# Kernel tuning notes

Measured on AMD Instinct MI355X. Metric: run time of the kernel, lower is better.

Reference implementation:

```python
import jax, jax.numpy as jnp
import numpy as np

D_MODEL = 1024
D_STATE = 16
D_CONV = 4
EXPAND = 2
D_INNER = EXPAND * D_MODEL          # 2048
DT_RANK = D_MODEL // 16             # 64 (math.ceil(d_model/16))
BATCH, SEQLEN = 2, 1024


def setup_inputs() -> dict:
    key = jax.random.key(0)
    ks = jax.random.split(key, 9)
    f32 = jnp.float32
    hidden_states = jax.random.normal(ks[0], (BATCH, SEQLEN, D_MODEL), dtype=f32)
    in_proj_w = jax.random.normal(ks[1], (2 * D_INNER, D_MODEL), dtype=f32) * (D_MODEL ** -0.5)
    conv1d_w = jax.random.normal(ks[2], (D_INNER, D_CONV), dtype=f32) * (D_CONV ** -0.5)
    conv1d_b = jax.random.normal(ks[3], (D_INNER,), dtype=f32) * 0.1
    x_proj_w = jax.random.normal(ks[4], (DT_RANK + 2 * D_STATE, D_INNER), dtype=f32) * (D_INNER ** -0.5)
    dt_std = DT_RANK ** -0.5
    dt_proj_w = jax.random.uniform(ks[5], (D_INNER, DT_RANK), dtype=f32, minval=-dt_std, maxval=dt_std)
    dt_proj_b = jax.random.normal(ks[6], (D_INNER,), dtype=f32) * 0.1
    # A = repeat(arange(1, d_state+1), 'n -> d n'); A_log = log(A)
    A_log = jnp.log(jnp.tile(jnp.arange(1, D_STATE + 1, dtype=f32), (D_INNER, 1)))
    D_param = jnp.ones((D_INNER,), dtype=f32)
    out_proj_w = jax.random.normal(ks[7], (D_MODEL, D_INNER), dtype=f32) * (D_INNER ** -0.5)
    return dict(hidden_states=hidden_states, in_proj_w=in_proj_w, conv1d_w=conv1d_w,
                conv1d_b=conv1d_b, x_proj_w=x_proj_w, dt_proj_w=dt_proj_w,
                dt_proj_b=dt_proj_b, A_log=A_log, D_param=D_param, out_proj_w=out_proj_w)


def _mamba_fwd(hidden_states, in_proj_w, conv1d_w, conv1d_b, x_proj_w,
               dt_proj_w, dt_proj_b, A_log, D_param, out_proj_w):
    Bsz, L, _ = hidden_states.shape
    # in_proj: (B,L,d_model) -> (B,L,2*d_inner); split into x, z
    xz = jnp.einsum('bld,ed->ble', hidden_states, in_proj_w)
    x, z = jnp.split(xz, 2, axis=-1)                      # each (B,L,d_inner)
    # causal depthwise conv1d over L (left pad d_conv-1), then SiLU (fused in causal_conv1d_fwd)
    xc = jnp.transpose(x, (0, 2, 1))                      # (B,d_inner,L)
    kern = conv1d_w[:, None, :]                           # (d_inner,1,d_conv)
    conv = jax.lax.conv_general_dilated(
        xc, kern, window_strides=(1,), padding=[(D_CONV - 1, 0)],
        dimension_numbers=('NCH', 'OIH', 'NCH'), feature_group_count=D_INNER)
    u = jax.nn.silu(conv + conv1d_b[None, :, None])       # (B,d_inner,L)
    ut = jnp.transpose(u, (0, 2, 1))                      # (B,L,d_inner)
    # x_proj -> [dt | B | C]
    x_dbl = jnp.einsum('bld,rd->blr', ut, x_proj_w)       # (B,L,dt_rank+2*d_state)
    dt_low = x_dbl[..., :DT_RANK]
    B_var = x_dbl[..., DT_RANK:DT_RANK + D_STATE]         # (B,L,d_state)
    C_var = x_dbl[..., DT_RANK + D_STATE:]                # (B,L,d_state)
    # delta = softplus(dt_proj_w @ dt_low + dt_proj_b)  (delta_bias applied inside selective scan)
    delta = jax.nn.softplus(jnp.einsum('blr,dr->bld', dt_low, dt_proj_w) + dt_proj_b)  # (B,L,d_inner)
    A = -jnp.exp(A_log)                                   # (d_inner,d_state)
    # discretize: h_l = exp(delta*A) * h_{l-1} + (delta*B_l) * u_l
    dA = jnp.exp(delta[..., None] * A)                    # (B,L,d_inner,d_state)
    dBu = delta[..., None] * B_var[:, :, None, :] * ut[..., None]  # (B,L,d_inner,d_state)

    def step(h, inp):
        da, dbu, c = inp
        h = da * h + dbu                                  # (B,d_inner,d_state)
        y = jnp.einsum('bdn,bn->bd', h, c)
        return h, y

    h0 = jnp.zeros((Bsz, D_INNER, D_STATE), dtype=hidden_states.dtype)
    _, ys = jax.lax.scan(step, h0, (jnp.moveaxis(dA, 1, 0),
                                    jnp.moveaxis(dBu, 1, 0),
                                    jnp.moveaxis(C_var, 1, 0)))
    y = jnp.moveaxis(ys, 0, 1)                            # (B,L,d_inner)
    y = y + ut * D_param                                  # skip term D*u
    out_z = y * jax.nn.silu(z)                            # gated output
    return jnp.einsum('bld,ed->ble', out_z, out_proj_w)   # (B,L,d_model)


def reference(hidden_states, in_proj_w, conv1d_w, conv1d_b, x_proj_w,
              dt_proj_w, dt_proj_b, A_log, D_param, out_proj_w):
    return _mamba_fwd(hidden_states, in_proj_w, conv1d_w, conv1d_b, x_proj_w,
                      dt_proj_w, dt_proj_b, A_log, D_param, out_proj_w)
```

## Files before the change

kernel.cpp:

```cpp
#include <hip/hip_runtime.h>
#include <hip/hip_bf16.h>

#define BATCH 2
#define SEQLEN 1024
#define DMODEL 1024
#define DINNER 2048
#define DSTATE 16
#define DTRANK 64
#define ROWS (BATCH * SEQLEN)
#define LOG2E 1.44269504088896340736f

using bf16 = __hip_bfloat16;
typedef __bf16 bf16x8 __attribute__((ext_vector_type(8)));
typedef float f32x4 __attribute__((ext_vector_type(4)));
typedef unsigned short us8 __attribute__((ext_vector_type(8)));

__device__ __forceinline__ float to_f(float x) { return x; }
__device__ __forceinline__ float to_f(bf16 x) { return __bfloat162float(x); }

__device__ __forceinline__ float fexp2(float x) { return __builtin_amdgcn_exp2f(x); }

__device__ __forceinline__ float bfu(unsigned short u) {
    union { unsigned int i; float f; } v;
    v.i = ((unsigned int)u) << 16;
    return v.f;
}

__device__ __forceinline__ unsigned short bf_bits(float x) {
    bf16 h = __float2bfloat16(x);
    union { bf16 b; unsigned short u; } cv;
    cv.b = h;
    return cv.u;
}

__device__ __forceinline__ float softplus_f(float x) {
    return fmaxf(x, 0.f) + log1pf(expf(-fabsf(x)));
}
__device__ __forceinline__ float silu_f(float x) {
    return x * __builtin_amdgcn_rcpf(1.f + fexp2(-x * LOG2E));
}

template <int CTRL>
__device__ __forceinline__ float dpp_shr(float x) {
    int r = __builtin_amdgcn_update_dpp(0, __builtin_bit_cast(int, x), CTRL, 0xF, 0xF, false);
    return __builtin_bit_cast(float, r);
}
__device__ __forceinline__ float row16_sum_to_lane15(float p) {
    p += dpp_shr<0x111>(p);
    p += dpp_shr<0x112>(p);
    p += dpp_shr<0x114>(p);
    p += dpp_shr<0x118>(p);
    return p;
}

__device__ __forceinline__ void gload16(const void* g, void* l) {
    __builtin_amdgcn_global_load_lds(
        (const __attribute__((address_space(1))) void*)g,
        (__attribute__((address_space(3))) void*)l, 16, 0, 0);
}

__global__ __launch_bounds__(256) void prep_kernel(const unsigned short* hs, int* flag,
                                                   float* zbuf, int nzero) {
    if (blockIdx.x == 0) {
        __shared__ int cnt[256];
        int c = 0;
        for (int i = threadIdx.x; i < 8192; i += 256) {
            int e = (hs[i] >> 7) & 0xFF;
            if (e == 0 || e == 0xFF || e < 96 || e > 159) c++;
        }
        cnt[threadIdx.x] = c;
        __syncthreads();
        for (int s = 128; s > 0; s >>= 1) {
            if (threadIdx.x < s) cnt[threadIdx.x] += cnt[threadIdx.x + s];
            __syncthreads();
        }
        if (threadIdx.x == 0) *flag = (cnt[0] < 512) ? 1 : 0;
    } else {
        int i = (blockIdx.x - 1) * 256 + threadIdx.x;
        if (i < nzero) zbuf[i] = 0.f;
    }
}

struct SrcPtrs { const void* p[10]; };

__device__ __constant__ const size_t SEG_OFF[11] = {
    0, 2097152, 6291456, 6299648, 6301696, 6498304,
    6629376, 6631424, 6664192, 6666240, 8763392
};

__global__ __launch_bounds__(256) void convert_all(SrcPtrs s, bf16* __restrict__ dst,
                                                   const int* __restrict__ flag) {
    size_t e = ((size_t)blockIdx.x * 256 + threadIdx.x) * 4;
    if (e >= SEG_OFF[10]) return;
    int seg = 0;
    #pragma unroll
    for (int i = 1; i < 10; ++i) if (e >= SEG_OFF[i]) seg = i;
    int isbf = *flag;
    if (isbf && (seg == 0 || seg == 1 || seg == 9)) return;
    size_t loc = e - SEG_OFF[seg];
    if (isbf) {
        ushort4 v = ((const ushort4*)s.p[seg])[loc / 4];
        ((ushort4*)(dst + e))[0] = v;
    } else {
        float4 v = ((const float4*)s.p[seg])[loc / 4];
        ushort4 o;
        o.x = bf_bits(v.x); o.y = bf_bits(v.y);
        o.z = bf_bits(v.z); o.w = bf_bits(v.w);
        ((ushort4*)(dst + e))[0] = o;
    }
}

template <int OUTMODE>
__global__ __launch_bounds__(256) void gemm_mfma(
    const bf16* __restrict__ A, int lda,
    const bf16* __restrict__ Bm, int ldb,
    void* __restrict__ C, int ldc,
    int Kspl, size_t pstride,
    const bf16* __restrict__ bias,
    const bf16* __restrict__ Aalt,
    const bf16* __restrict__ Balt,
    const int* __restrict__ flag)
{
    if (flag && *flag) {
        if (Aalt) A = Aalt;
        if (Balt) Bm = Balt;
    }
    __shared__ __align__(16) __bf16 sA[128 * 32];
    __shared__ __align__(16) __bf16 sB[128 * 32];
    const int tid = threadIdx.x;
    const int m0 = blockIdx.y * 128;
    const int n0 = blockIdx.x * 128;
    const int wid = tid >> 6, ln = tid & 63;
    const int wy = (wid >> 1) * 64, wx = (wid & 1) * 64;
    const int q = ln >> 4, m16 = ln & 15;
    const int kbeg = blockIdx.z * Kspl;

    f32x4 acc[4][4] = {};

    for (int k0 = kbeg; k0 < kbeg + Kspl; k0 += 32) {
        #pragma unroll
        for (int i = 0; i < 2; ++i) {
            int idx = tid + i * 256;
            int r = idx >> 2, c = (idx & 3) * 8;
            gload16(&A[(size_t)(m0 + r) * lda + k0 + c], &sA[idx * 8]);
        }
        #pragma unroll
        for (int i = 0; i < 2; ++i) {
            int idx = tid + i * 256;
            int r = idx >> 2, c = (idx & 3) * 8;
            gload16(&Bm[(size_t)(n0 + r) * ldb + k0 + c], &sB[idx * 8]);
        }
        __syncthreads();
        bf16x8 a[4], b[4];
        #pragma unroll
        for (int i = 0; i < 4; ++i)
            a[i] = *(const bf16x8*)&sA[(wy + i * 16 + m16) * 32 + q * 8];
        #pragma unroll
        for (int j = 0; j < 4; ++j)
            b[j] = *(const bf16x8*)&sB[(wx + j * 16 + m16) * 32 + q * 8];
        #pragma unroll
        for (int i = 0; i < 4; ++i)
            #pragma unroll
            for (int j = 0; j < 4; ++j)
                acc[i][j] = __builtin_amdgcn_mfma_f32_16x16x32_bf16(a[i], b[j], acc[i][j], 0, 0, 0);
        __syncthreads();
    }

    #pragma unroll
    for (int i = 0; i < 4; ++i) {
        #pragma unroll
        for (int j = 0; j < 4; ++j) {
            #pragma unroll
            for (int r = 0; r < 4; ++r) {
                int row = m0 + wy + i * 16 + q * 4 + r;
                int col = n0 + wx + j * 16 + m16;
                size_t idx = (size_t)row * ldc + col;
                float v = acc[i][j][r];
                if constexpr (OUTMODE == 0) {
                    ((bf16*)C)[idx] = __float2bfloat16(v);
                } else if constexpr (OUTMODE == 2) {
                    ((float*)C + blockIdx.z * pstride)[idx] = v;
                } else if constexpr (OUTMODE == 3) {
                    if (col < 96) atomicAdd((float*)C + idx, v);
                } else if constexpr (OUTMODE == 4) {
                    ((float*)C)[idx] = softplus_f(v + to_f(bias[row]));
                }
            }
        }
    }
}

__global__ __launch_bounds__(256) void sum_store(
    const float* __restrict__ p0, const float* __restrict__ p1,
    void* __restrict__ out, const int* __restrict__ flag, int n4)
{
    int i = blockIdx.x * 256 + threadIdx.x;
    if (i >= n4) return;
    float4 a = ((const float4*)p0)[i];
    float4 b = ((const float4*)p1)[i];
    float4 sv; sv.x = a.x + b.x; sv.y = a.y + b.y; sv.z = a.z + b.z; sv.w = a.w + b.w;
    if (*flag) {
        ushort4 o;
        o.x = bf_bits(sv.x); o.y = bf_bits(sv.y);
        o.z = bf_bits(sv.z); o.w = bf_bits(sv.w);
        ((ushort4*)out)[i] = o;
    } else {
        ((float4*)out)[i] = sv;
    }
}

__global__ __launch_bounds__(256) void transpose_bf16(
    const ushort* __restrict__ src,
    ushort* __restrict__ dst)
{
    __shared__ ushort t[64][65];
    const int bx = blockIdx.x;
    const int by = blockIdx.y;
    const int tid = threadIdx.x;
    const int lr = tid & 63;
    const int ld = tid >> 6;
    #pragma unroll
    for (int i = 0; i < 16; ++i) {
        int d = ld + i * 4;
        t[d][lr] = src[(size_t)(by * 64 + d) * ROWS + bx * 64 + lr];
    }
    __syncthreads();
    #pragma unroll
    for (int i = 0; i < 16; ++i) {
        int r = ld + i * 4;
        dst[(size_t)(bx * 64 + r) * DINNER + by * 64 + lr] = t[lr][r];
    }
}

__global__ __launch_bounds__(256) void xd_post(
    const float* __restrict__ xd,
    float* __restrict__ xdT,
    bf16* __restrict__ xd_bf)
{
    __shared__ float t[96][65];
    const int row0 = blockIdx.x * 64;
    const int tid = threadIdx.x;
    for (int i = tid; i < 64 * 96; i += 256) {
        int row = i / 96, r = i - row * 96;
        float v = xd[(size_t)(row0 + row) * 96 + r];
        t[r][row] = v;
        xd_bf[(size_t)(row0 + row) * 96 + r] = __float2bfloat16(v);
    }
    __syncthreads();
    for (int i = tid; i < 96 * 64; i += 256) {
        int r = i >> 6, row = i & 63;
        xdT[(size_t)r * ROWS + row0 + row] = t[r][row];
    }
}

__global__ __launch_bounds__(256) void conv_silu_T8(
    const bf16* __restrict__ xzT,
    const bf16* __restrict__ w,
    const bf16* __restrict__ bias,
    bf16* __restrict__ utT)
{
    int t = blockIdx.x * 256 + threadIdx.x;
    int r0 = (t * 8) & (ROWS - 1);
    int d = t >> 8;

    const ushort* xp = (const ushort*)xzT + (size_t)d * ROWS + r0;
    float x[11];
    us8 cur = *(const us8*)xp;
    #pragma unroll
    for (int j = 0; j < 8; ++j) x[3 + j] = bfu(cur[j]);
    if ((r0 & (SEQLEN - 1)) != 0) {
        ushort4 pv = *(const ushort4*)(xp - 4);
        x[0] = bfu(pv.y); x[1] = bfu(pv.z); x[2] = bfu(pv.w);
    } else {
        x[0] = x[1] = x[2] = 0.f;
    }

    ushort4 wv = *(const ushort4*)((const ushort*)w + d * 4);
    float w0 = bfu(wv.x), w1 = bfu(wv.y), w2 = bfu(wv.z), w3 = bfu(wv.w);
    float bv = to_f(bias[d]);

    us8 o;
    #pragma unroll
    for (int j = 0; j < 8; ++j) {
        float acc = bv;
        acc = fmaf(x[j],     w0, acc);
        acc = fmaf(x[j + 1], w1, acc);
        acc = fmaf(x[j + 2], w2, acc);
        acc = fmaf(x[j + 3], w3, acc);
        o[j] = bf_bits(silu_f(acc));
    }
    *(us8*)((ushort*)utT + (size_t)d * ROWS + r0) = o;
}

#define SCHUNK 16
#define SSTEPS (SEQLEN / SCHUNK)
__global__ __launch_bounds__(1024) void scan_kernel11(
    const float* __restrict__ deltaT,
    const bf16*  __restrict__ utT,
    const float* __restrict__ xdT,
    const bf16*  __restrict__ xzT,
    const bf16*  __restrict__ A_log,
    const bf16*  __restrict__ Dp,
    bf16* __restrict__ outzT)
{
    __shared__ float sH[SCHUNK][64], sP[SCHUNK][64];
    const int tid = threadIdx.x;
    const int c = tid >> 6;
    const int w = tid & 63;
    const int n = tid & 15;
    const int b = blockIdx.x >> 9;
    const int d = ((blockIdx.x & 511) << 2) + ((tid >> 4) & 3);
    const int row0 = b * SEQLEN + c * SSTEPS;

    const float Aa2 = -expf(to_f(A_log[d * DSTATE + n])) * LOG2E;
    const float Dv = to_f(Dp[d]);

    const float*  dp = deltaT + (size_t)d * ROWS + row0;
    const ushort* up = (const ushort*)utT + (size_t)d * ROWS + row0;
    const ushort* zp = (const ushort*)xzT + (size_t)(DINNER + d) * ROWS + row0;
    const float*  Bp = xdT + (size_t)(64 + n) * ROWS + row0;
    const float*  Cp = xdT + (size_t)(80 + n) * ROWS + row0;

    float h = 0.f, sd = 0.f;
    for (int i0 = 0; i0 < SSTEPS; i0 += 4) {
        float4  dv4 = *(const float4*)(dp + i0);
        ushort4 uv4 = *(const ushort4*)(up + i0);
        float4  Bv4 = *(const float4*)(Bp + i0);
        float dv[4] = {dv4.x, dv4.y, dv4.z, dv4.w};
        float uv[4] = {bfu(uv4.x), bfu(uv4.y), bfu(uv4.z), bfu(uv4.w)};
        float Bv[4] = {Bv4.x, Bv4.y, Bv4.z, Bv4.w};
        #pragma unroll
        for (int j = 0; j < 4; ++j) {
            float a = fexp2(dv[j] * Aa2);
            h = fmaf(a, h, dv[j] * Bv[j] * uv[j]);
            sd += dv[j];
        }
    }
    sH[c][w] = h;
    sP[c][w] = fexp2(sd * Aa2);
    __syncthreads();

    float hin = 0.f;
    for (int cc = 0; cc < c; ++cc)
        hin = fmaf(sP[cc][w], hin, sH[cc][w]);

    h = hin;
    for (int i0 = 0; i0 < SSTEPS; i0 += 4) {
        float4  dv4 = *(const float4*)(dp + i0);
        ushort4 uv4 = *(const ushort4*)(up + i0);
        float4  Bv4 = *(const float4*)(Bp + i0);
        float4  Cv4 = *(const float4*)(Cp + i0);
        ushort4 zv4 = *(const ushort4*)(zp + i0);
        float dv[4] = {dv4.x, dv4.y, dv4.z, dv4.w};
        float uv[4] = {bfu(uv4.x), bfu(uv4.y), bfu(uv4.z), bfu(uv4.w)};
        float Bv[4] = {Bv4.x, Bv4.y, Bv4.z, Bv4.w};
        float Cv[4] = {Cv4.x, Cv4.y, Cv4.z, Cv4.w};
        float zv[4] = {bfu(zv4.x), bfu(zv4.y), bfu(zv4.z), bfu(zv4.w)};
        float y[4];
        #pragma unroll
        for (int j = 0; j < 4; ++j) {
            float a = fexp2(dv[j] * Aa2);
            h = fmaf(a, h, dv[j] * Bv[j] * uv[j]);
            float p = h * Cv[j];
            p = row16_sum_to_lane15(p);
            y[j] = fmaf(uv[j], Dv, p);
        }
        if (n == 15) {
            ushort4 o;
            o.x = bf_bits(y[0] * silu_f(zv[0]));
            o.y = bf_bits(y[1] * silu_f(zv[1]));
            o.z = bf_bits(y[2] * silu_f(zv[2]));
            o.w = bf_bits(y[3] * silu_f(zv[3]));
            *(ushort4*)((ushort*)outzT + (size_t)d * ROWS + row0 + i0) = o;
        }
    }
}

extern "C" void kernel_launch(void* const* d_in, const int* in_sizes, int n_in,
                              void* d_out, int out_size, void* d_ws, size_t ws_size,
                              hipStream_t stream) {
    static const size_t SZ[10] = {
        (size_t)BATCH * SEQLEN * DMODEL,
        (size_t)2 * DINNER * DMODEL,
        (size_t)DINNER * 4,
        (size_t)DINNER,
        (size_t)(DTRANK + 2 * DSTATE) * DINNER,
        (size_t)DINNER * DTRANK,
        (size_t)DINNER,
        (size_t)DINNER * DSTATE,
        (size_t)DINNER,
        (size_t)DMODEL * DINNER
    };
    size_t tot_in = 0;
    for (int i = 0; i < 10; ++i) tot_in += SZ[i];

    char* p = (char*)d_ws;
    int* flag = (int*)p;                     p += 64;
    bf16* inb = (bf16*)p;                    p += tot_in * 2;
    bf16* xzT = (bf16*)p;                    p += (size_t)4096 * ROWS * 2;
    bf16* utT = (bf16*)p;                    p += (size_t)DINNER * ROWS * 2;
    bf16* ut  = (bf16*)p;                    p += (size_t)ROWS * DINNER * 2;
    float* xd = (float*)p;                   p += (size_t)ROWS * 96 * 4;
    bf16* xd_bf = (bf16*)p;                  p += (size_t)ROWS * 96 * 2;
    float* xdT = (float*)p;                  p += (size_t)96 * ROWS * 4;
    float* deltaT = (float*)p;               p += (size_t)DINNER * ROWS * 4;
    bf16* outzT = (bf16*)p;                  p += (size_t)DINNER * ROWS * 2;
    bf16* outz = (bf16*)p;                   p += (size_t)ROWS * DINNER * 2;
    float* part = (float*)p;                 p += (size_t)2 * ROWS * DMODEL * 4;
    size_t needed = (size_t)(p - (char*)d_ws);
    if (ws_size < needed) return;

    dim3 blk(256);

    prep_kernel<<<1 + (ROWS * 96 + 255) / 256, blk, 0, stream>>>(
        (const unsigned short*)d_in[0], flag, xd, ROWS * 96);

    bf16* inp[10];
    {
        size_t off = 0;
        for (int i = 0; i < 10; ++i) { inp[i] = inb + off; off += SZ[i]; }
    }
    SrcPtrs sp;
    for (int i = 0; i < 10; ++i) sp.p[i] = d_in[i];
    convert_all<<<(int)((tot_in / 4 + 255) / 256), blk, 0, stream>>>(sp, inb, flag);

    const bf16* hs        = inp[0];
    const bf16* in_proj_w = inp[1];
    const bf16* conv_w    = inp[2];
    const bf16* conv_b    = inp[3];
    const bf16* x_proj_w  = inp[4];
    const bf16* dt_proj_w = inp[5];
    const bf16* dt_proj_b = inp[6];
    const bf16* A_log     = inp[7];
    const bf16* Dp        = inp[8];
    const bf16* out_proj_w= inp[9];

    gemm_mfma<0><<<dim3(ROWS / 128, 4096 / 128, 1), blk, 0, stream>>>(
        in_proj_w, DMODEL, hs, DMODEL, xzT, ROWS, DMODEL, 0, nullptr,
        (const bf16*)d_in[1], (const bf16*)d_in[0], flag);

    conv_silu_T8<<<(DINNER * ROWS / 8) / 256, blk, 0, stream>>>(xzT, conv_w, conv_b, utT);

    transpose_bf16<<<dim3(ROWS / 64, DINNER / 64), blk, 0, stream>>>(
        (const ushort*)utT, (ushort*)ut);

    gemm_mfma<3><<<dim3(1, ROWS / 128, 4), blk, 0, stream>>>(
        ut, DINNER, x_proj_w, DINNER, xd, 96, DINNER / 4, 0, nullptr,
        nullptr, nullptr, nullptr);

    xd_post<<<ROWS / 64, blk, 0, stream>>>(xd, xdT, xd_bf);

    gemm_mfma<4><<<dim3(ROWS / 128, DINNER / 128, 1), blk, 0, stream>>>(
        dt_proj_w, DTRANK, xd_bf, 96, deltaT, ROWS, DTRANK, 0, dt_proj_b,
        nullptr, nullptr, nullptr);

    scan_kernel11<<<BATCH * (DINNER / 4), dim3(1024), 0, stream>>>(
        deltaT, utT, xdT, xzT, A_log, Dp, outzT);

    transpose_bf16<<<dim3(ROWS / 64, DINNER / 64), blk, 0, stream>>>(
        (const ushort*)outzT, (ushort*)outz);

    gemm_mfma<2><<<dim3(DMODEL / 128, ROWS / 128, 2), blk, 0, stream>>>(
        outz, DINNER, out_proj_w, DINNER, part, DMODEL, DINNER / 2, (size_t)ROWS * DMODEL,
        nullptr, nullptr, (const bf16*)d_in[9], flag);

    sum_store<<<(ROWS * DMODEL / 4 + 255) / 256, blk, 0, stream>>>(
        part, part + (size_t)ROWS * DMODEL, d_out, flag, ROWS * DMODEL / 4);
}
```

Baseline: 348.7 us.

## Reuse first-pass local scan outputs and apply carry-in correction via cumulative decay

The first scan pass now computes per-chunk local outputs (zero initial state) and cumulative delta sums, storing them in shared memory. The second pass adds the carry-in state's contribution using exp(A*cumsum(delta)) instead of rerunning the recurrence, so delta, u and B are not reloaded. Next-iteration loads are prefetched. This costs more shared memory and moves the reduction work into the first pass, and the prefetch reads slightly past each chunk's range.

```diff
diff --git a/kernel.cpp b/kernel.cpp
--- a/kernel.cpp
+++ b/kernel.cpp
@@ -294,7 +294,7 @@
 
 #define SCHUNK 16
 #define SSTEPS (SEQLEN / SCHUNK)
-__global__ __launch_bounds__(1024) void scan_kernel11(
+__global__ __launch_bounds__(1024) void scan_kernel12(
     const float* __restrict__ deltaT,
     const bf16*  __restrict__ utT,
     const float* __restrict__ xdT,
@@ -304,12 +304,15 @@
     bf16* __restrict__ outzT)
 {
     __shared__ float sH[SCHUNK][64], sP[SCHUNK][64];
+    __shared__ float sQ[SCHUNK][4][68];
+    __shared__ float sS[SCHUNK][4][68];
     const int tid = threadIdx.x;
     const int c = tid >> 6;
     const int w = tid & 63;
+    const int dcol = (tid >> 4) & 3;
     const int n = tid & 15;
     const int b = blockIdx.x >> 9;
-    const int d = ((blockIdx.x & 511) << 2) + ((tid >> 4) & 3);
+    const int d = ((blockIdx.x & 511) << 2) + dcol;
     const int row0 = b * SEQLEN + c * SSTEPS;
 
     const float Aa2 = -expf(to_f(A_log[d * DSTATE + n])) * LOG2E;
@@ -321,49 +324,65 @@
     const float*  Bp = xdT + (size_t)(64 + n) * ROWS + row0;
     const float*  Cp = xdT + (size_t)(80 + n) * ROWS + row0;
 
-    float h = 0.f, sd = 0.f;
+    float hl = 0.f, sd = 0.f;
+    float4  dv4 = *(const float4*)(dp);
+    ushort4 uv4 = *(const ushort4*)(up);
+    float4  Bv4 = *(const float4*)(Bp);
+    float4  Cv4 = *(const float4*)(Cp);
     for (int i0 = 0; i0 < SSTEPS; i0 += 4) {
-        float4  dv4 = *(const float4*)(dp + i0);
-        ushort4 uv4 = *(const ushort4*)(up + i0);
-        float4  Bv4 = *(const float4*)(Bp + i0);
-        float dv[4] = {dv4.x, dv4.y, dv4.z, dv4.w};
-        float uv[4] = {bfu(uv4.x), bfu(uv4.y), bfu(uv4.z), bfu(uv4.w)};
-        float Bv[4] = {Bv4.x, Bv4.y, Bv4.z, Bv4.w};
-        #pragma unroll
-        for (int j = 0; j < 4; ++j) {
-            float a = fexp2(dv[j] * Aa2);
-            h = fmaf(a, h, dv[j] * Bv[j] * uv[j]);
-            sd += dv[j];
-        }
-    }
-    sH[c][w] = h;
-    sP[c][w] = fexp2(sd * Aa2);
-    __syncthreads();
-
-    float hin = 0.f;
-    for (int cc = 0; cc < c; ++cc)
-        hin = fmaf(sP[cc][w], hin, sH[cc][w]);
-
-    h = hin;
-    for (int i0 = 0; i0 < SSTEPS; i0 += 4) {
-        float4  dv4 = *(const float4*)(dp + i0);
-        ushort4 uv4 = *(const ushort4*)(up + i0);
-        float4  Bv4 = *(const float4*)(Bp + i0);
-        float4  Cv4 = *(const float4*)(Cp + i0);
-        ushort4 zv4 = *(const ushort4*)(zp + i0);
+        float4  dvn = *(const float4*)(dp + i0 + 4);
+        ushort4 uvn = *(const ushort4*)(up + i0 + 4);
+        float4  Bvn = *(const float4*)(Bp + i0 + 4);
+        float4  Cvn = *(const float4*)(Cp + i0 + 4);
         float dv[4] = {dv4.x, dv4.y, dv4.z, dv4.w};
         float uv[4] = {bfu(uv4.x), bfu(uv4.y), bfu(uv4.z), bfu(uv4.w)};
         float Bv[4] = {Bv4.x, Bv4.y, Bv4.z, Bv4.w};
         float Cv[4] = {Cv4.x, Cv4.y, Cv4.z, Cv4.w};
+        float qv[4], sv[4];
+        #pragma unroll
+        for (int j = 0; j < 4; ++j) {
+            sd += dv[j];
+            sv[j] = sd;
+            float a = fexp2(dv[j] * Aa2);
+            hl = fmaf(a, hl, dv[j] * Bv[j] * uv[j]);
+            float p = hl * Cv[j];
+            p = row16_sum_to_lane15(p);
+            qv[j] = fmaf(uv[j], Dv, p);
+        }
+        if (n == 15) {
+            float4 qo; qo.x = qv[0]; qo.y = qv[1]; qo.z = qv[2]; qo.w = qv[3];
+            float4 so; so.x = sv[0]; so.y = sv[1]; so.z = sv[2]; so.w = sv[3];
+            *(float4*)&sQ[c][dcol][i0] = qo;
+            *(float4*)&sS[c][dcol][i0] = so;
+        }
+        dv4 = dvn; uv4 = uvn; Bv4 = Bvn; Cv4 = Cvn;
+    }
+    sH[c][w] = hl;
+    sP[c][w] = fexp2(sd * Aa2);
+    __syncthreads();
+
+    float hin = 0.f;
+    for (int cc = 0; cc < c; ++cc)
+        hin = fmaf(sP[cc][w], hin, sH[cc][w]);
+
+    ushort4 zv4 = *(const ushort4*)(zp);
+    float4  Cw4 = *(const float4*)(Cp);
+    for (int i0 = 0; i0 < SSTEPS; i0 += 4) {
+        ushort4 zvn = *(const ushort4*)(zp + i0 + 4);
+        float4  Cwn = *(const float4*)(Cp + i0 + 4);
+        float4 q4 = *(const float4*)&sQ[c][dcol][i0];
+        float4 s4 = *(const float4*)&sS[c][dcol][i0];
+        float Cv[4] = {Cw4.x, Cw4.y, Cw4.z, Cw4.w};
+        float ss[4] = {s4.x, s4.y, s4.z, s4.w};
+        float qq[4] = {q4.x, q4.y, q4.z, q4.w};
         float zv[4] = {bfu(zv4.x), bfu(zv4.y), bfu(zv4.z), bfu(zv4.w)};
         float y[4];
         #pragma unroll
         for (int j = 0; j < 4; ++j) {
-            float a = fexp2(dv[j] * Aa2);
-            h = fmaf(a, h, dv[j] * Bv[j] * uv[j]);
-            float p = h * Cv[j];
+            float e = fexp2(ss[j] * Aa2);
+            float p = (hin * e) * Cv[j];
             p = row16_sum_to_lane15(p);
-            y[j] = fmaf(uv[j], Dv, p);
+            y[j] = qq[j] + p;
         }
         if (n == 15) {
             ushort4 o;
@@ -373,6 +392,7 @@
             o.w = bf_bits(y[3] * silu_f(zv[3]));
             *(ushort4*)((ushort*)outzT + (size_t)d * ROWS + row0 + i0) = o;
         }
+        zv4 = zvn; Cw4 = Cwn;
     }
 }
 
@@ -454,7 +474,7 @@
         dt_proj_w, DTRANK, xd_bf, 96, deltaT, ROWS, DTRANK, 0, dt_proj_b,
         nullptr, nullptr, nullptr);
 
-    scan_kernel11<<<BATCH * (DINNER / 4), dim3(1024), 0, stream>>>(
+    scan_kernel12<<<BATCH * (DINNER / 4), dim3(1024), 0, stream>>>(
         deltaT, utT, xdT, xzT, A_log, Dp, outzT);
 
     transpose_bf16<<<dim3(ROWS / 64, DINNER / 64), blk, 0, stream>>>(
```

After: 342.7 us. No clear change (-1.7%).
